# Optimization experiments

Hardware: AMD Instinct MI355X
Metric: run time of the kernel (lower is better)

Reference implementation:

```python
import jax, jax.numpy as jnp
import numpy as np


def setup_inputs() -> dict:
    key = jax.random.key(0)
    B, C, H, W = 8, 64, 64, 64
    x = jax.random.normal(key, (B, C, H, W), dtype=jnp.float32)
    return {"x": x}


def reference(x) -> jnp.ndarray:
    # x: (B, C, H, W). Spatial self-attention over N = H*W positions with
    # Q = K = V = flattened x, no scaling, no projections (the Conv2d in the
    # original __init__ is never used in forward).
    B, C, H, W = x.shape
    N = H * W
    f = x.reshape(B, C, N)  # (B, C, N)
    # att[b, n, m] = sum_c f[b, c, n] * f[b, c, m]  -> (B, N, N)
    att = jnp.einsum('bcn,bcm->bnm', f, f)
    att = jax.nn.softmax(att, axis=-1)
    # outp[b, c, n] = sum_m f[b, c, m] * att[b, n, m]^T  (f_x @ att)
    outp = jnp.einsum('bcm,bmn->bcn', f, att).reshape(B, C, H, W)
    return x + outp
```

## Files before the change

### kernel.cpp

```cpp
#include <hip/hip_runtime.h>

typedef short v8s __attribute__((ext_vector_type(8)));
typedef float v4f __attribute__((ext_vector_type(4)));

#define LOG2E 1.44269504088896340736f

#define WS_FBF_T 0u
#define WS_FVP   4194304u
#define WS_G     8388608u
#define WS_BMAX  8519680u
#define WS_NEED  8521728u

__device__ __forceinline__ unsigned short f2bf_rne(float f) {
  unsigned int u = __builtin_bit_cast(unsigned int, f);
  u += 0x7FFFu + ((u >> 16) & 1u);
  return (unsigned short)(u >> 16);
}

__device__ __forceinline__ unsigned int pack_hi16(float hi, float lo) {
#if defined(__has_builtin) && __has_builtin(__builtin_amdgcn_perm)
  return __builtin_amdgcn_perm(__builtin_bit_cast(unsigned int, hi),
                               __builtin_bit_cast(unsigned int, lo), 0x07060302u);
#else
  return (__builtin_bit_cast(unsigned int, hi) & 0xFFFF0000u) |
         (__builtin_bit_cast(unsigned int, lo) >> 16);
#endif
}

__global__ __launch_bounds__(256) void prep_kernel(
    const float* __restrict__ x, unsigned short* __restrict__ fbf_t,
    unsigned short* __restrict__ fvp, float* __restrict__ g, float* __restrict__ bmax) {
  __shared__ float red[4][64];
  const int t = threadIdx.x;
  const int b = blockIdx.x >> 6, ch = blockIdx.x & 63;
  const int n0 = ch << 6, nn = t & 63, n = n0 + nn, cg = t >> 6;

  const int kin = nn & 31;
  const int slot = (kin < 16) ? (((kin >> 2) << 3) + (kin & 3))
                              : ((((kin - 16) >> 2) << 3) + ((kin - 16) & 3) + 4);
  const int ncol = (n & ~31) + slot;

  float sq = 0.f;
  unsigned short w[16];
#pragma unroll
  for (int j = 0; j < 16; ++j) {
    const int c = cg * 16 + j;
    float v = x[((size_t)(b * 64 + c) << 12) + n];
    sq = __builtin_fmaf(v, v, sq);
    w[j] = f2bf_rne(v);
  }
  unsigned short* ft = fbf_t + ((size_t)b << 18) + (size_t)n * 64 + cg * 16;
  *(v8s*)ft = *(v8s*)&w[0];
  *(v8s*)(ft + 8) = *(v8s*)&w[8];
#pragma unroll
  for (int j = 0; j < 16; ++j)
    fvp[((size_t)(b * 64 + cg * 16 + j) << 12) + ncol] = w[j];

  red[cg][nn] = sq;
  __syncthreads();
  if (t < 64) {
    float tot = (red[0][t] + red[1][t]) + (red[2][t] + red[3][t]);
    g[b * 4096 + n0 + t] = tot;
    float m = tot;
    m = fmaxf(m, __shfl_xor(m, 1, 64));
    m = fmaxf(m, __shfl_xor(m, 2, 64));
    m = fmaxf(m, __shfl_xor(m, 4, 64));
    m = fmaxf(m, __shfl_xor(m, 8, 64));
    m = fmaxf(m, __shfl_xor(m, 16, 64));
    m = fmaxf(m, __shfl_xor(m, 32, 64));
    if (t == 0) bmax[b * 64 + ch] = m;
  }
}

__global__ __launch_bounds__(512, 4) void chanattn_main(
    const float* __restrict__ x, const unsigned short* __restrict__ fbf_t,
    const unsigned short* __restrict__ fvp, const float* __restrict__ g,
    const float* __restrict__ bmax, float* __restrict__ out) {
  __shared__ __align__(16) unsigned char smem[73728];
  unsigned short* sKtB = (unsigned short*)smem;
  unsigned short* sVcB = (unsigned short*)(smem + 18432);
  float* lred = (float*)(smem + 71680);
  const int BUF = 17920;

  const int tid = threadIdx.x;
  const int wave = tid >> 6, lane = tid & 63, quad = lane >> 4, l15 = lane & 15;
  const int qg = wave >> 2, kg = wave & 3;
  const int b = blockIdx.x >> 6, qt = blockIdx.x & 63;

  const unsigned short* fT = fbf_t + ((size_t)b << 18);
  const unsigned short* fV = fvp + ((size_t)b << 18);

  const int sKey = tid >> 3, sC = (tid & 7) << 3;
  const int vC = tid >> 4, vK = (tid & 15) << 3;

  float gm = bmax[b * 64 + lane];
  gm = fmaxf(gm, __shfl_xor(gm, 1, 64));
  gm = fmaxf(gm, __shfl_xor(gm, 2, 64));
  gm = fmaxf(gm, __shfl_xor(gm, 4, 64));
  gm = fmaxf(gm, __shfl_xor(gm, 8, 64));
  gm = fmaxf(gm, __shfl_xor(gm, 16, 64));
  gm = fmaxf(gm, __shfl_xor(gm, 32, 64));
  float gq[2];
#pragma unroll
  for (int jq = 0; jq < 2; ++jq)
    gq[jq] = g[b * 4096 + qt * 64 + qg * 32 + jq * 16 + l15];

  *(v8s*)&sKtB[sKey * 72 + sC] =
      *(const v8s*)&fT[(size_t)(qt * 64 + sKey) * 64 + sC];
  v8s pfk[2], pfv[2];
#pragma unroll
  for (int i = 0; i < 2; ++i)
    pfk[i] = *(const v8s*)&fT[(size_t)(sKey + i * 64) * 64 + sC];
#pragma unroll
  for (int i = 0; i < 2; ++i)
    pfv[i] = *(const v8s*)&fV[(size_t)(vC + i * 32) * 4096 + vK];

  __syncthreads();
  v8s bQ[2][2];
#pragma unroll
  for (int jq = 0; jq < 2; ++jq)
#pragma unroll
    for (int cs = 0; cs < 2; ++cs)
      bQ[jq][cs] = *(const v8s*)&sKtB[(qg * 32 + jq * 16 + l15) * 72 + cs * 32 + quad * 8];
  float msc[2];
#pragma unroll
  for (int jq = 0; jq < 2; ++jq) msc[jq] = __builtin_sqrtf(gq[jq] * gm) * LOG2E;
  __syncthreads();

#pragma unroll
  for (int i = 0; i < 2; ++i)
    *(v8s*)&sKtB[(sKey + i * 64) * 72 + sC] = pfk[i];
#pragma unroll
  for (int i = 0; i < 2; ++i)
    *(v8s*)&sVcB[(vC + i * 32) * 136 + vK] = pfv[i];
#pragma unroll
  for (int i = 0; i < 2; ++i)
    pfk[i] = *(const v8s*)&fT[(size_t)(128 + sKey + i * 64) * 64 + sC];
#pragma unroll
  for (int i = 0; i < 2; ++i)
    pfv[i] = *(const v8s*)&fV[(size_t)(vC + i * 32) * 4096 + 128 + vK];

  v4f oacc[4][2];
  float rsum[2];
#pragma unroll
  for (int ct = 0; ct < 4; ++ct)
#pragma unroll
    for (int jq = 0; jq < 2; ++jq) oacc[ct][jq] = (v4f){0.f, 0.f, 0.f, 0.f};
#pragma unroll
  for (int jq = 0; jq < 2; ++jq) rsum[jq] = 0.f;

  for (int kt = 0; kt < 32; ++kt) {
    __syncthreads();
    const int po = (kt & 1) * BUF;
    const int pn = ((kt & 1) ^ 1) * BUF;

    v8s aK[2][2];
#pragma unroll
    for (int t = 0; t < 2; ++t)
#pragma unroll
      for (int cs = 0; cs < 2; ++cs)
        aK[t][cs] =
            *(const v8s*)&sKtB[po + (kg * 32 + t * 16 + l15) * 72 + cs * 32 + quad * 8];
    v8s aV[4];
#pragma unroll
    for (int ct = 0; ct < 4; ++ct)
      aV[ct] = *(const v8s*)&sVcB[po + (ct * 16 + l15) * 136 + kg * 32 + quad * 8];

    {
      const int jq = 0;
      v4f s0 = (v4f){0.f, 0.f, 0.f, 0.f}, s1 = (v4f){0.f, 0.f, 0.f, 0.f};
#pragma unroll
      for (int cs = 0; cs < 2; ++cs) {
        s0 = __builtin_amdgcn_mfma_f32_16x16x32_bf16(aK[0][cs], bQ[jq][cs], s0, 0, 0, 0);
        s1 = __builtin_amdgcn_mfma_f32_16x16x32_bf16(aK[1][cs], bQ[jq][cs], s1, 0, 0, 0);
      }
      float p0[4], p1[4];
#pragma unroll
      for (int r = 0; r < 4; ++r) {
        p0[r] = __builtin_amdgcn_exp2f(__builtin_fmaf(s0[r], LOG2E, -msc[jq]));
        p1[r] = __builtin_amdgcn_exp2f(__builtin_fmaf(s1[r], LOG2E, -msc[jq]));
      }
      rsum[jq] += ((p0[0] + p0[1]) + (p0[2] + p0[3])) +
                  ((p1[0] + p1[1]) + (p1[2] + p1[3]));
      uint4 up;
      up.x = pack_hi16(p0[1], p0[0]);
      up.y = pack_hi16(p0[3], p0[2]);
      up.z = pack_hi16(p1[1], p1[0]);
      up.w = pack_hi16(p1[3], p1[2]);
      v8s bp = __builtin_bit_cast(v8s, up);
#pragma unroll
      for (int ct = 0; ct < 4; ++ct)
        oacc[ct][jq] =
            __builtin_amdgcn_mfma_f32_16x16x32_bf16(aV[ct], bp, oacc[ct][jq], 0, 0, 0);
    }

    if (kt < 31) {
#pragma unroll
      for (int i = 0; i < 2; ++i)
        *(v8s*)&sKtB[pn + (sKey + i * 64) * 72 + sC] = pfk[i];
#pragma unroll
      for (int i = 0; i < 2; ++i)
        *(v8s*)&sVcB[pn + (vC + i * 32) * 136 + vK] = pfv[i];
    }
    if (kt < 30) {
      const int k0 = (kt + 2) << 7;
#pragma unroll
      for (int i = 0; i < 2; ++i)
        pfk[i] = *(const v8s*)&fT[(size_t)(k0 + sKey + i * 64) * 64 + sC];
#pragma unroll
      for (int i = 0; i < 2; ++i)
        pfv[i] = *(const v8s*)&fV[(size_t)(vC + i * 32) * 4096 + k0 + vK];
    }

#pragma unroll
    for (int jq = 1; jq < 2; ++jq) {
      v4f s0 = (v4f){0.f, 0.f, 0.f, 0.f}, s1 = (v4f){0.f, 0.f, 0.f, 0.f};
#pragma unroll
      for (int cs = 0; cs < 2; ++cs) {
        s0 = __builtin_amdgcn_mfma_f32_16x16x32_bf16(aK[0][cs], bQ[jq][cs], s0, 0, 0, 0);
        s1 = __builtin_amdgcn_mfma_f32_16x16x32_bf16(aK[1][cs], bQ[jq][cs], s1, 0, 0, 0);
      }
      float p0[4], p1[4];
#pragma unroll
      for (int r = 0; r < 4; ++r) {
        p0[r] = __builtin_amdgcn_exp2f(__builtin_fmaf(s0[r], LOG2E, -msc[jq]));
        p1[r] = __builtin_amdgcn_exp2f(__builtin_fmaf(s1[r], LOG2E, -msc[jq]));
      }
      rsum[jq] += ((p0[0] + p0[1]) + (p0[2] + p0[3])) +
                  ((p1[0] + p1[1]) + (p1[2] + p1[3]));
      uint4 up;
      up.x = pack_hi16(p0[1], p0[0]);
      up.y = pack_hi16(p0[3], p0[2]);
      up.z = pack_hi16(p1[1], p1[0]);
      up.w = pack_hi16(p1[3], p1[2]);
      v8s bp = __builtin_bit_cast(v8s, up);
#pragma unroll
      for (int ct = 0; ct < 4; ++ct)
        oacc[ct][jq] =
            __builtin_amdgcn_mfma_f32_16x16x32_bf16(aV[ct], bp, oacc[ct][jq], 0, 0, 0);
    }
  }

#pragma unroll
  for (int jq = 0; jq < 2; ++jq) {
    float s = rsum[jq];
    s += __shfl_xor(s, 16, 64);
    s += __shfl_xor(s, 32, 64);
    rsum[jq] = s;
  }
  if (quad == 0) {
#pragma unroll
    for (int jq = 0; jq < 2; ++jq)
      lred[(qg * 32 + jq * 16 + l15) * 4 + kg] = rsum[jq];
  }
  __syncthreads();
  float inv[2];
#pragma unroll
  for (int jq = 0; jq < 2; ++jq) {
    const float4 lv = *(const float4*)&lred[(qg * 32 + jq * 16 + l15) * 4];
    inv[jq] = __builtin_amdgcn_rcpf((lv.x + lv.y) + (lv.z + lv.w));
  }

  float* Obuf = (float*)smem;
#pragma unroll
  for (int round = 0; round < 4; ++round) {
    if (kg == round) {
#pragma unroll
      for (int ct = 0; ct < 4; ++ct)
#pragma unroll
        for (int jq = 0; jq < 2; ++jq)
#pragma unroll
          for (int r = 0; r < 4; ++r) {
            float val = oacc[ct][jq][r] * inv[jq];
            float* p = &Obuf[(ct * 16 + quad * 4 + r) * 68 + qg * 32 + jq * 16 + l15];
            if (round == 0) *p = val; else *p += val;
          }
    }
    __syncthreads();
  }
#pragma unroll
  for (int j = 0; j < 2; ++j) {
    int idx = tid + j * 512;
    int c = idx >> 4, q4 = idx & 15;
    const float4 o = *(const float4*)&Obuf[c * 68 + q4 * 4];
    size_t gidx = ((size_t)(b * 64 + c) << 12) + (unsigned)(qt * 64 + q4 * 4);
    const float4 xv = *(const float4*)(x + gidx);
    float4 rv;
    rv.x = xv.x + o.x; rv.y = xv.y + o.y; rv.z = xv.z + o.z; rv.w = xv.w + o.w;
    *(float4*)(out + gidx) = rv;
  }
}

__global__ __launch_bounds__(512) void
chanattn_fallback(const float* __restrict__ x, float* __restrict__ out) {
  __shared__ __align__(16) unsigned char smem[54272];
  unsigned short* sKt = (unsigned short*)smem;
  unsigned short* sVc = (unsigned short*)(smem + 18432);
  unsigned short* sP  = (unsigned short*)(smem + 35840);
  const int tid = threadIdx.x;
  const int wave = tid >> 6, lane = tid & 63, quad = lane >> 4, l15 = lane & 15;
  const int b = blockIdx.x & 7, qt = blockIdx.x >> 3;
  const float* fb = x + (size_t)b * (64 * 4096);
  const int skey = tid & 127, sc0 = (tid >> 7) << 4;
  {
    float vq[16];
#pragma unroll
    for (int j = 0; j < 16; ++j) vq[j] = fb[(sc0 + j) * 4096 + qt * 128 + skey];
    unsigned short us[16];
#pragma unroll
    for (int j = 0; j < 16; ++j) us[j] = f2bf_rne(vq[j]);
#pragma unroll
    for (int h = 0; h < 2; ++h) {
      v8s t;
#pragma unroll
      for (int j = 0; j < 8; ++j) t[j] = (short)us[h * 8 + j];
      *(v8s*)&sKt[skey * 72 + sc0 + h * 8] = t;
    }
  }
  float vk[16];
#pragma unroll
  for (int j = 0; j < 16; ++j) vk[j] = fb[(sc0 + j) * 4096 + skey];
  __syncthreads();
  v8s aq[2];
#pragma unroll
  for (int cs = 0; cs < 2; ++cs)
    aq[cs] = *(const v8s*)&sKt[(wave * 16 + l15) * 72 + cs * 32 + quad * 8];
  __syncthreads();
  v4f oacc[4];
#pragma unroll
  for (int ct = 0; ct < 4; ++ct) oacc[ct] = (v4f){0.f, 0.f, 0.f, 0.f};
  float m_run[4], l_run[4];
#pragma unroll
  for (int r = 0; r < 4; ++r) { m_run[r] = -3.0e38f; l_run[r] = 0.f; }
  unsigned short* sPw = sP + wave * (16 * 72);
  for (int kt = 0; kt < 32; ++kt) {
    {
      unsigned short us[16];
#pragma unroll
      for (int j = 0; j < 16; ++j) us[j] = f2bf_rne(vk[j]);
#pragma unroll
      for (int h = 0; h < 2; ++h) {
        v8s t;
#pragma unroll
        for (int j = 0; j < 8; ++j) t[j] = (short)us[h * 8 + j];
        *(v8s*)&sKt[skey * 72 + sc0 + h * 8] = t;
      }
#pragma unroll
      for (int j = 0; j < 16; ++j) sVc[(sc0 + j) * 136 + skey] = us[j];
    }
    __syncthreads();
    if (kt + 1 < 32) {
      const int m0 = (kt + 1) * 128;
#pragma unroll
      for (int j = 0; j < 16; ++j) vk[j] = fb[(sc0 + j) * 4096 + m0 + skey];
    }
    v4f sacc[8];
#pragma unroll
    for (int t = 0; t < 8; ++t) {
      v4f acc = (v4f){0.f, 0.f, 0.f, 0.f};
#pragma unroll
      for (int cs = 0; cs < 2; ++cs) {
        v8s bf = *(const v8s*)&sKt[(t * 16 + l15) * 72 + cs * 32 + quad * 8];
        acc = __builtin_amdgcn_mfma_f32_16x16x32_bf16(aq[cs], bf, acc, 0, 0, 0);
      }
      sacc[t] = acc;
    }
    float alpha[4], msc[4], rsum[4];
#pragma unroll
    for (int r = 0; r < 4; ++r) {
      float mv = sacc[0][r];
#pragma unroll
      for (int t = 1; t < 8; ++t) mv = fmaxf(mv, sacc[t][r]);
      mv = fmaxf(mv, __shfl_xor(mv, 8, 64));
      mv = fmaxf(mv, __shfl_xor(mv, 4, 64));
      mv = fmaxf(mv, __shfl_xor(mv, 2, 64));
      mv = fmaxf(mv, __shfl_xor(mv, 1, 64));
      float mnew = fmaxf(m_run[r], mv);
      alpha[r] = __builtin_amdgcn_exp2f((m_run[r] - mnew) * LOG2E);
      m_run[r] = mnew;
      msc[r] = mnew * LOG2E;
      l_run[r] *= alpha[r];
      rsum[r] = 0.f;
    }
#pragma unroll
    for (int ct = 0; ct < 4; ++ct)
#pragma unroll
      for (int r = 0; r < 4; ++r) oacc[ct][r] *= alpha[r];
#pragma unroll
    for (int half = 0; half < 2; ++half) {
#pragma unroll
      for (int t = half * 4; t < half * 4 + 4; ++t)
#pragma unroll
        for (int r = 0; r < 4; ++r) {
          float p = __builtin_amdgcn_exp2f(__builtin_fmaf(sacc[t][r], LOG2E, -msc[r]));
          rsum[r] += p;
          sPw[(quad * 4 + r) * 72 + (t - half * 4) * 16 + l15] = f2bf_rne(p);
        }
      asm volatile("s_waitcnt lgkmcnt(0)" ::: "memory");
#pragma unroll
      for (int ms = 0; ms < 2; ++ms) {
        v8s af = *(const v8s*)&sPw[l15 * 72 + ms * 32 + quad * 8];
#pragma unroll
        for (int ct = 0; ct < 4; ++ct) {
          v8s bf = *(const v8s*)&sVc[(ct * 16 + l15) * 136 + (half * 2 + ms) * 32 + quad * 8];
          oacc[ct] = __builtin_amdgcn_mfma_f32_16x16x32_bf16(af, bf, oacc[ct], 0, 0, 0);
        }
      }
      asm volatile("s_waitcnt lgkmcnt(0)" ::: "memory");
    }
#pragma unroll
    for (int r = 0; r < 4; ++r) {
      float s = rsum[r];
      s += __shfl_xor(s, 8, 64);
      s += __shfl_xor(s, 4, 64);
      s += __shfl_xor(s, 2, 64);
      s += __shfl_xor(s, 1, 64);
      l_run[r] += s;
    }
    __syncthreads();
  }
  float inv[4];
#pragma unroll
  for (int r = 0; r < 4; ++r) inv[r] = __builtin_amdgcn_rcpf(l_run[r]);
  float* sOt = (float*)smem;
#pragma unroll
  for (int ct = 0; ct < 4; ++ct)
#pragma unroll
    for (int r = 0; r < 4; ++r)
      sOt[(ct * 16 + l15) * 132 + wave * 16 + quad * 4 + r] = oacc[ct][r] * inv[r];
  __syncthreads();
#pragma unroll
  for (int j = 0; j < 4; ++j) {
    int idx = tid + j * 512;
    int nv = idx & 31, c = idx >> 5;
    float4 o = *(const float4*)&sOt[c * 132 + nv * 4];
    size_t gaddr = (size_t)b * (64 * 4096) + (size_t)c * 4096 + (size_t)(qt * 128 + nv * 4);
    float4 xv = *(const float4*)(x + gaddr);
    float4 res = make_float4(xv.x + o.x, xv.y + o.y, xv.z + o.z, xv.w + o.w);
    *(float4*)(out + gaddr) = res;
  }
}

extern "C" void kernel_launch(void* const* d_in, const int* in_sizes, int n_in,
                              void* d_out, int out_size, void* d_ws, size_t ws_size,
                              hipStream_t stream) {
  const float* xin = (const float*)d_in[0];
  float* out = (float*)d_out;
  if (ws_size >= (size_t)WS_NEED) {
    unsigned short* fbf_t = (unsigned short*)((char*)d_ws + WS_FBF_T);
    unsigned short* fvp = (unsigned short*)((char*)d_ws + WS_FVP);
    float* g = (float*)((char*)d_ws + WS_G);
    float* bmax = (float*)((char*)d_ws + WS_BMAX);
    prep_kernel<<<dim3(512), dim3(256), 0, stream>>>(xin, fbf_t, fvp, g, bmax);
    chanattn_main<<<dim3(512), dim3(512), 0, stream>>>(xin, fbf_t, fvp, g, bmax, out);
  } else {
    chanattn_fallback<<<dim3(256), dim3(512), 0, stream>>>(xin, out);
  }
}
```

Measured before the change: 107.9 us.

## Double the query tile per block to 128 using 1024-thread blocks

Each block now runs 16 waves and handles 128 query positions instead of 64, so every K/V tile staged in shared memory is reused by twice as many query rows. Each thread now prefetches one K and one V vector per step instead of two, and the grid is halved to 256 blocks. The epilogue reduction buffer is indexed by query half so the 128-wide output tile fits. In exchange the register budget per thread may tighten under the new launch bounds, and with fewer, larger blocks there is less freedom to schedule blocks across CUs.

```diff
diff --git a/kernel.cpp b/kernel.cpp
--- a/kernel.cpp
+++ b/kernel.cpp
@@ -72,7 +72,7 @@
   }
 }
 
-__global__ __launch_bounds__(512, 4) void chanattn_main(
+__global__ __launch_bounds__(1024, 4) void chanattn_main(
     const float* __restrict__ x, const unsigned short* __restrict__ fbf_t,
     const unsigned short* __restrict__ fvp, const float* __restrict__ g,
     const float* __restrict__ bmax, float* __restrict__ out) {
@@ -85,7 +85,7 @@
   const int tid = threadIdx.x;
   const int wave = tid >> 6, lane = tid & 63, quad = lane >> 4, l15 = lane & 15;
   const int qg = wave >> 2, kg = wave & 3;
-  const int b = blockIdx.x >> 6, qt = blockIdx.x & 63;
+  const int b = blockIdx.x >> 5, qt = blockIdx.x & 31;
 
   const unsigned short* fT = fbf_t + ((size_t)b << 18);
   const unsigned short* fV = fvp + ((size_t)b << 18);
@@ -103,17 +103,13 @@
   float gq[2];
 #pragma unroll
   for (int jq = 0; jq < 2; ++jq)
-    gq[jq] = g[b * 4096 + qt * 64 + qg * 32 + jq * 16 + l15];
+    gq[jq] = g[b * 4096 + qt * 128 + qg * 32 + jq * 16 + l15];
 
   *(v8s*)&sKtB[sKey * 72 + sC] =
-      *(const v8s*)&fT[(size_t)(qt * 64 + sKey) * 64 + sC];
-  v8s pfk[2], pfv[2];
-#pragma unroll
-  for (int i = 0; i < 2; ++i)
-    pfk[i] = *(const v8s*)&fT[(size_t)(sKey + i * 64) * 64 + sC];
-#pragma unroll
-  for (int i = 0; i < 2; ++i)
-    pfv[i] = *(const v8s*)&fV[(size_t)(vC + i * 32) * 4096 + vK];
+      *(const v8s*)&fT[(size_t)(qt * 128 + sKey) * 64 + sC];
+  v8s pfk, pfv;
+  pfk = *(const v8s*)&fT[(size_t)sKey * 64 + sC];
+  pfv = *(const v8s*)&fV[(size_t)vC * 4096 + vK];
 
   __syncthreads();
   v8s bQ[2][2];
@@ -127,18 +123,10 @@
   for (int jq = 0; jq < 2; ++jq) msc[jq] = __builtin_sqrtf(gq[jq] * gm) * LOG2E;
   __syncthreads();
 
-#pragma unroll
-  for (int i = 0; i < 2; ++i)
-    *(v8s*)&sKtB[(sKey + i * 64) * 72 + sC] = pfk[i];
-#pragma unroll
-  for (int i = 0; i < 2; ++i)
-    *(v8s*)&sVcB[(vC + i * 32) * 136 + vK] = pfv[i];
-#pragma unroll
-  for (int i = 0; i < 2; ++i)
-    pfk[i] = *(const v8s*)&fT[(size_t)(128 + sKey + i * 64) * 64 + sC];
-#pragma unroll
-  for (int i = 0; i < 2; ++i)
-    pfv[i] = *(const v8s*)&fV[(size_t)(vC + i * 32) * 4096 + 128 + vK];
+  *(v8s*)&sKtB[sKey * 72 + sC] = pfk;
+  *(v8s*)&sVcB[vC * 136 + vK] = pfv;
+  pfk = *(const v8s*)&fT[(size_t)(128 + sKey) * 64 + sC];
+  pfv = *(const v8s*)&fV[(size_t)vC * 4096 + 128 + vK];
 
   v4f oacc[4][2];
   float rsum[2];
@@ -195,21 +183,13 @@
     }
 
     if (kt < 31) {
-#pragma unroll
-      for (int i = 0; i < 2; ++i)
-        *(v8s*)&sKtB[pn + (sKey + i * 64) * 72 + sC] = pfk[i];
-#pragma unroll
-      for (int i = 0; i < 2; ++i)
-        *(v8s*)&sVcB[pn + (vC + i * 32) * 136 + vK] = pfv[i];
+      *(v8s*)&sKtB[pn + sKey * 72 + sC] = pfk;
+      *(v8s*)&sVcB[pn + vC * 136 + vK] = pfv;
     }
     if (kt < 30) {
       const int k0 = (kt + 2) << 7;
-#pragma unroll
-      for (int i = 0; i < 2; ++i)
-        pfk[i] = *(const v8s*)&fT[(size_t)(k0 + sKey + i * 64) * 64 + sC];
-#pragma unroll
-      for (int i = 0; i < 2; ++i)
-        pfv[i] = *(const v8s*)&fV[(size_t)(vC + i * 32) * 4096 + k0 + vK];
+      pfk = *(const v8s*)&fT[(size_t)(k0 + sKey) * 64 + sC];
+      pfv = *(const v8s*)&fV[(size_t)vC * 4096 + k0 + vK];
     }
 
 #pragma unroll
@@ -272,7 +252,8 @@
 #pragma unroll
           for (int r = 0; r < 4; ++r) {
             float val = oacc[ct][jq][r] * inv[jq];
-            float* p = &Obuf[(ct * 16 + quad * 4 + r) * 68 + qg * 32 + jq * 16 + l15];
+            float* p = &Obuf[((qg >> 1) * 64 + ct * 16 + quad * 4 + r) * 68 +
+                             (qg & 1) * 32 + jq * 16 + l15];
             if (round == 0) *p = val; else *p += val;
           }
     }
@@ -280,10 +261,10 @@
   }
 #pragma unroll
   for (int j = 0; j < 2; ++j) {
-    int idx = tid + j * 512;
-    int c = idx >> 4, q4 = idx & 15;
-    const float4 o = *(const float4*)&Obuf[c * 68 + q4 * 4];
-    size_t gidx = ((size_t)(b * 64 + c) << 12) + (unsigned)(qt * 64 + q4 * 4);
+    int idx = tid + j * 1024;
+    int qg2 = idx >> 10, c = (idx >> 4) & 63, q4 = idx & 15;
+    const float4 o = *(const float4*)&Obuf[(qg2 * 64 + c) * 68 + q4 * 4];
+    size_t gidx = ((size_t)(b * 64 + c) << 12) + (unsigned)(qt * 128 + qg2 * 64 + q4 * 4);
     const float4 xv = *(const float4*)(x + gidx);
     float4 rv;
     rv.x = xv.x + o.x; rv.y = xv.y + o.y; rv.z = xv.z + o.z; rv.w = xv.w + o.w;
@@ -452,7 +433,7 @@
     float* g = (float*)((char*)d_ws + WS_G);
     float* bmax = (float*)((char*)d_ws + WS_BMAX);
     prep_kernel<<<dim3(512), dim3(256), 0, stream>>>(xin, fbf_t, fvp, g, bmax);
-    chanattn_main<<<dim3(512), dim3(512), 0, stream>>>(xin, fbf_t, fvp, g, bmax, out);
+    chanattn_main<<<dim3(256), dim3(1024), 0, stream>>>(xin, fbf_t, fvp, g, bmax, out);
   } else {
     chanattn_fallback<<<dim3(256), dim3(512), 0, stream>>>(xin, out);
   }
```

Result: faster. 103.2 us (-4.3%).
